# Kernel tuning notes

Measured on AMD Instinct MI355X. Metric: run time of the kernel, lower is better.

The kernel has to match this reference:

```python
import jax, jax.numpy as jnp
import numpy as np

B, T, D = 4, 2048, 1024
H = 16
HD = D // H  # 64


def setup_inputs() -> dict:
    key = jax.random.key(0)
    ks = jax.random.split(key, 6)
    s = 0.02
    x = jax.random.normal(ks[0], (B, T, D), dtype=jnp.float32)
    # per-head projection weights, stored stacked: [H, HD, D] (torch Linear weight layout)
    Wq = jax.random.normal(ks[1], (H, HD, D), dtype=jnp.float32) * s
    Wk = jax.random.normal(ks[2], (H, HD, D), dtype=jnp.float32) * s
    Wv = jax.random.normal(ks[3], (H, HD, D), dtype=jnp.float32) * s
    Wo = jax.random.normal(ks[4], (D, D), dtype=jnp.float32) * s  # proj weight [out, in]
    bo = jax.random.normal(ks[5], (D,), dtype=jnp.float32) * s
    return {"x": x, "Wq": Wq, "Wk": Wk, "Wv": Wv, "Wo": Wo, "bo": bo}


def reference(x, Wq, Wk, Wv, Wo, bo):
    Bx, Tx, _ = x.shape
    # project: [B,T,D] x [H,HD,D] -> [B,H,T,HD]
    q = jnp.einsum('btd,hed->bhte', x, Wq)
    k = jnp.einsum('btd,hed->bhte', x, Wk)
    v = jnp.einsum('btd,hed->bhte', x, Wv)
    scale = 1.0 / jnp.sqrt(jnp.array(q.shape[-1], dtype=x.dtype))
    scores = jnp.einsum('bhte,bhse->bhts', q, k) * scale  # [B,H,T,T]
    causal = jnp.tril(jnp.ones((Tx, Tx), dtype=bool))
    scores = jnp.where(causal, scores, jnp.array(-jnp.inf, dtype=scores.dtype))
    weights = jax.nn.softmax(scores, axis=-1)
    out = jnp.einsum('bhts,bhse->bhte', weights, v)  # [B,H,T,HD]
    # concat heads (head h occupies contiguous slice, matching torch.cat order)
    out = out.transpose(0, 2, 1, 3).reshape(Bx, Tx, -1)  # [B,T,D]
    out = out @ Wo.T + bo
    return out
```

## Files before the change

kernel.cpp:

```cpp
#include <hip/hip_runtime.h>
#include <cstdint>
#include <cstddef>

typedef unsigned short u16;
typedef float  f32x4  __attribute__((ext_vector_type(4)));
typedef __bf16 bf16x8 __attribute__((ext_vector_type(8)));
typedef unsigned short us8 __attribute__((ext_vector_type(8)));
typedef unsigned short us4 __attribute__((ext_vector_type(4)));
typedef float  f32x4v __attribute__((ext_vector_type(4)));

#define AS1 __attribute__((address_space(1)))
#define AS3 __attribute__((address_space(3)))

__device__ __forceinline__ u16 f2b(float f) {
  unsigned u = __float_as_uint(f);
  u += 0x7FFFu + ((u >> 16) & 1u);
  return (u16)(u >> 16);
}

__device__ __forceinline__ bf16x8 ldfrag(const u16* p) {
  us8 v = *(const us8*)p;
  return __builtin_bit_cast(bf16x8, v);
}

__device__ __forceinline__ f32x4 mfma16(bf16x8 a, bf16x8 b, f32x4 c) {
  return __builtin_amdgcn_mfma_f32_16x16x32_bf16(a, b, c, 0, 0, 0);
}

__device__ __forceinline__ void gl_lds16(const u16* g, AS3 u16* l) {
  __builtin_amdgcn_global_load_lds((AS1 void*)g, (AS3 void*)l, 16, 0, 0);
}

__global__ __launch_bounds__(256) void cvt_bf16(const float* __restrict__ s,
                                                u16* __restrict__ d, int n4) {
  int i = blockIdx.x * 256 + threadIdx.x;
  if (i >= n4) return;
  f32x4v f = ((const f32x4v*)s)[i];
  us4 o = { f2b(f[0]), f2b(f[1]), f2b(f[2]), f2b(f[3]) };
  ((us4*)d)[i] = o;
}

__global__ __launch_bounds__(256) void gemm_qkv(
    const u16* __restrict__ A, const u16* __restrict__ W,
    u16* __restrict__ Qb, u16* __restrict__ Kb, u16* __restrict__ Vt) {
  __shared__ u16 lA[128 * 32];
  __shared__ u16 lB[128 * 32];
  const int tid = threadIdx.x;
  const int lane = tid & 63, wave = tid >> 6;
  const int quad = lane >> 4, l16 = lane & 15;
  const int wr = wave >> 1, wc = wave & 1;
  const int m0 = blockIdx.y * 128;
  const int n0 = blockIdx.x * 128;
  const int sec = n0 >> 10;
  AS3 u16* lA3 = (AS3 u16*)lA;
  AS3 u16* lB3 = (AS3 u16*)lB;
  f32x4 acc[4][4] = {};
  const int c0 = tid, c1 = tid + 256;
  const int ar0 = m0 + (c0 >> 2), ac0 = (c0 & 3) * 8;
  const int ar1 = m0 + (c1 >> 2), ac1 = (c1 & 3) * 8;
  const int br0 = n0 + (c0 >> 2);
  const int br1 = n0 + (c1 >> 2);

  for (int k0 = 0; k0 < 1024; k0 += 32) {
    __syncthreads();
    gl_lds16(A + (size_t)ar0 * 1024 + k0 + ac0, lA3 + wave * 512);
    gl_lds16(A + (size_t)ar1 * 1024 + k0 + ac1, lA3 + 2048 + wave * 512);
    gl_lds16(W + (size_t)br0 * 1024 + k0 + ac0, lB3 + wave * 512);
    gl_lds16(W + (size_t)br1 * 1024 + k0 + ac1, lB3 + 2048 + wave * 512);
    __syncthreads();
    bf16x8 aF[4], bF[4];
#pragma unroll
    for (int mt = 0; mt < 4; mt++)
      aF[mt] = ldfrag(&lA[(wr * 64 + mt * 16 + l16) * 32 + quad * 8]);
#pragma unroll
    for (int nt = 0; nt < 4; nt++)
      bF[nt] = ldfrag(&lB[(wc * 64 + nt * 16 + l16) * 32 + quad * 8]);
    if (sec != 2) {
#pragma unroll
      for (int mt = 0; mt < 4; mt++)
#pragma unroll
        for (int nt = 0; nt < 4; nt++)
          acc[mt][nt] = mfma16(aF[mt], bF[nt], acc[mt][nt]);
    } else {
#pragma unroll
      for (int mt = 0; mt < 4; mt++)
#pragma unroll
        for (int nt = 0; nt < 4; nt++)
          acc[mt][nt] = mfma16(bF[nt], aF[mt], acc[mt][nt]);
    }
  }

  if (sec != 2) {
#pragma unroll
    for (int mt = 0; mt < 4; mt++) {
#pragma unroll
      for (int nt = 0; nt < 4; nt++) {
#pragma unroll
        for (int r = 0; r < 4; r++) {
          float v = acc[mt][nt][r];
          int m = m0 + wr * 64 + mt * 16 + quad * 4 + r;
          int n = n0 + wc * 64 + nt * 16 + l16;
          int ns = n & 1023;
          int h = ns >> 6, e = ns & 63;
          int b = m >> 11, t = m & 2047;
          size_t bh = (size_t)b * 16 + h;
          if (sec == 0) Qb[(bh * 2048 + t) * 64 + e] = f2b(v * 0.125f);
          else          Kb[(bh * 2048 + t) * 64 + e] = f2b(v);
        }
      }
    }
  } else {
#pragma unroll
    for (int mt = 0; mt < 4; mt++) {
#pragma unroll
      for (int nt = 0; nt < 4; nt++) {
#pragma unroll
        for (int r = 0; r < 4; r++) {
          float v = acc[mt][nt][r];
          int n = n0 + wc * 64 + nt * 16 + quad * 4 + r;
          int m = m0 + wr * 64 + mt * 16 + l16;
          int ns = n & 1023;
          int h = ns >> 6, e = ns & 63;
          int b = m >> 11, t = m & 2047;
          size_t bh = (size_t)b * 16 + h;
          Vt[(bh * 64 + e) * 2048 + t] = f2b(v);
        }
      }
    }
  }
}

__global__ __launch_bounds__(512, 4) void attn(
    const u16* __restrict__ Q, const u16* __restrict__ K,
    const u16* __restrict__ Vt, u16* __restrict__ O) {
  __shared__ u16 lK[128 * 72];
  __shared__ u16 lV[64 * 136];
  __shared__ u16 lP[8 * 16 * 40];
  const int tid = threadIdx.x;
  const int lane = tid & 63, wave = tid >> 6;
  const int quad = lane >> 4, l16 = lane & 15;
  const int bh = blockIdx.x;
  const int qb = 15 - (int)blockIdx.y;
  const int t0 = qb << 7;
  const size_t base = (size_t)bh * (2048 * 64);
  u16* lPw = lP + wave * 640;

  const int tq = t0 + wave * 16 + l16;
  const bf16x8 qF0 = ldfrag(Q + base + (size_t)tq * 64 + quad * 8);
  const bf16x8 qF1 = ldfrag(Q + base + (size_t)tq * 64 + 32 + quad * 8);

  float m_i = -INFINITY, l_i = 0.f;
  f32x4 o[4] = {};

  for (int j = 0; j <= qb; j++) {
    const int s0 = j << 7;
    __syncthreads();
#pragma unroll
    for (int i = 0; i < 2; i++) {
      int c = tid + i * 512;
      int r = c >> 3, col = (c & 7) * 8;
      *(us8*)&lK[r * 72 + col] = *(const us8*)(K + base + (size_t)(s0 + r) * 64 + col);
    }
#pragma unroll
    for (int i = 0; i < 2; i++) {
      int c = tid + i * 512;
      int e = c >> 4, col = (c & 15) * 8;
      *(us8*)&lV[e * 136 + col] = *(const us8*)(Vt + base + (size_t)e * 2048 + s0 + col);
    }
    __syncthreads();

    f32x4 S[8];
#pragma unroll
    for (int nt = 0; nt < 8; nt++) {
      int sr = nt * 16 + l16;
      f32x4 a = {};
      a = mfma16(ldfrag(&lK[sr * 72 + quad * 8]), qF0, a);
      a = mfma16(ldfrag(&lK[sr * 72 + 32 + quad * 8]), qF1, a);
      S[nt] = a;
    }

    if (j == qb) {
#pragma unroll
      for (int nt = 0; nt < 8; nt++)
#pragma unroll
        for (int r = 0; r < 4; r++) {
          int s = s0 + nt * 16 + quad * 4 + r;
          if (s > tq) S[nt][r] = -INFINITY;
        }
    }

    f32x4 m4 = S[0];
#pragma unroll
    for (int nt = 1; nt < 8; nt++)
#pragma unroll
      for (int r = 0; r < 4; r++) m4[r] = fmaxf(m4[r], S[nt][r]);
    float mx = fmaxf(fmaxf(m4[0], m4[1]), fmaxf(m4[2], m4[3]));
    mx = fmaxf(mx, __shfl_xor(mx, 16));
    mx = fmaxf(mx, __shfl_xor(mx, 32));
    float mn = fmaxf(m_i, mx);
    float alpha = exp2f((m_i - mn) * 1.44269504f);
    float sum = 0.f;
#pragma unroll
    for (int nt = 0; nt < 8; nt++)
#pragma unroll
      for (int r = 0; r < 4; r++) {
        float p = exp2f((S[nt][r] - mn) * 1.44269504f);
        S[nt][r] = p;
        sum += p;
      }
    sum += __shfl_xor(sum, 16);
    sum += __shfl_xor(sum, 32);
    l_i = l_i * alpha + sum;
    m_i = mn;
#pragma unroll
    for (int ot = 0; ot < 4; ot++)
#pragma unroll
      for (int r = 0; r < 4; r++) o[ot][r] *= alpha;

#pragma unroll
    for (int c = 0; c < 4; c++) {
      us4 p0 = { f2b(S[2*c][0]),   f2b(S[2*c][1]),   f2b(S[2*c][2]),   f2b(S[2*c][3]) };
      us4 p1 = { f2b(S[2*c+1][0]), f2b(S[2*c+1][1]), f2b(S[2*c+1][2]), f2b(S[2*c+1][3]) };
      *(us4*)&lPw[l16 * 40 + quad * 4]      = p0;
      *(us4*)&lPw[l16 * 40 + 16 + quad * 4] = p1;
      __asm__ volatile("s_waitcnt lgkmcnt(0)" ::: "memory");
      bf16x8 bP = ldfrag(&lPw[l16 * 40 + quad * 8]);
#pragma unroll
      for (int ot = 0; ot < 4; ot++)
        o[ot] = mfma16(ldfrag(&lV[(ot * 16 + l16) * 136 + c * 32 + quad * 8]), bP, o[ot]);
    }
  }

  const float inv = 1.f / l_i;
  const int b = bh >> 4, h = bh & 15;
#pragma unroll
  for (int ot = 0; ot < 4; ot++) {
    us4 pk = { f2b(o[ot][0] * inv), f2b(o[ot][1] * inv),
               f2b(o[ot][2] * inv), f2b(o[ot][3] * inv) };
    *(us4*)&O[((size_t)b * 2048 + tq) * 1024 + h * 64 + ot * 16 + quad * 4] = pk;
  }
}

__global__ __launch_bounds__(256) void gemm_out(
    const u16* __restrict__ A, const u16* __restrict__ W,
    const float* __restrict__ bias, float* __restrict__ out) {
  __shared__ u16 lA[128 * 32];
  __shared__ u16 lB[128 * 32];
  const int tid = threadIdx.x;
  const int lane = tid & 63, wave = tid >> 6;
  const int quad = lane >> 4, l16 = lane & 15;
  const int wr = wave >> 1, wc = wave & 1;
  const int m0 = blockIdx.y * 128;
  const int n0 = blockIdx.x * 128;
  AS3 u16* lA3 = (AS3 u16*)lA;
  AS3 u16* lB3 = (AS3 u16*)lB;
  f32x4 acc[4][4] = {};
  const int c0 = tid, c1 = tid + 256;
  const int ar0 = m0 + (c0 >> 2), ac0 = (c0 & 3) * 8;
  const int ar1 = m0 + (c1 >> 2), ac1 = (c1 & 3) * 8;
  const int br0 = n0 + (c0 >> 2);
  const int br1 = n0 + (c1 >> 2);

  for (int k0 = 0; k0 < 1024; k0 += 32) {
    __syncthreads();
    gl_lds16(A + (size_t)ar0 * 1024 + k0 + ac0, lA3 + wave * 512);
    gl_lds16(A + (size_t)ar1 * 1024 + k0 + ac1, lA3 + 2048 + wave * 512);
    gl_lds16(W + (size_t)br0 * 1024 + k0 + ac0, lB3 + wave * 512);
    gl_lds16(W + (size_t)br1 * 1024 + k0 + ac1, lB3 + 2048 + wave * 512);
    __syncthreads();
    bf16x8 aF[4], bF[4];
#pragma unroll
    for (int mt = 0; mt < 4; mt++)
      aF[mt] = ldfrag(&lA[(wr * 64 + mt * 16 + l16) * 32 + quad * 8]);
#pragma unroll
    for (int nt = 0; nt < 4; nt++)
      bF[nt] = ldfrag(&lB[(wc * 64 + nt * 16 + l16) * 32 + quad * 8]);
#pragma unroll
    for (int mt = 0; mt < 4; mt++)
#pragma unroll
      for (int nt = 0; nt < 4; nt++)
        acc[mt][nt] = mfma16(aF[mt], bF[nt], acc[mt][nt]);
  }

#pragma unroll
  for (int mt = 0; mt < 4; mt++) {
#pragma unroll
    for (int nt = 0; nt < 4; nt++) {
#pragma unroll
      for (int r = 0; r < 4; r++) {
        int m = m0 + wr * 64 + mt * 16 + quad * 4 + r;
        int n = n0 + wc * 64 + nt * 16 + l16;
        out[(size_t)m * 1024 + n] = acc[mt][nt][r] + bias[n];
      }
    }
  }
}

extern "C" void kernel_launch(void* const* d_in, const int* in_sizes, int n_in,
                              void* d_out, int out_size, void* d_ws, size_t ws_size,
                              hipStream_t stream) {
  const float* x  = (const float*)d_in[0];
  const float* Wq = (const float*)d_in[1];
  const float* Wk = (const float*)d_in[2];
  const float* Wv = (const float*)d_in[3];
  const float* Wo = (const float*)d_in[4];
  const float* bo = (const float*)d_in[5];
  float* out = (float*)d_out;

  u16* ws   = (u16*)d_ws;
  u16* xb   = ws;
  u16* Wqkv = ws + 8388608;
  u16* Wob  = ws + 11534336;
  u16* Qb   = ws + 12582912;
  u16* Ao   = xb;
  u16* Kb   = (u16*)d_out;
  u16* Vt   = Kb + 8388608;

  cvt_bf16<<<8192, 256, 0, stream>>>(x, xb, 2097152);
  cvt_bf16<<<1024, 256, 0, stream>>>(Wq, Wqkv,            262144);
  cvt_bf16<<<1024, 256, 0, stream>>>(Wk, Wqkv + 1048576,  262144);
  cvt_bf16<<<1024, 256, 0, stream>>>(Wv, Wqkv + 2097152,  262144);
  cvt_bf16<<<1024, 256, 0, stream>>>(Wo, Wob,             262144);

  gemm_qkv<<<dim3(24, 64), 256, 0, stream>>>(xb, Wqkv, Qb, Kb, Vt);
  attn<<<dim3(64, 16), 512, 0, stream>>>(Qb, Kb, Vt, Ao);
  gemm_out<<<dim3(8, 64), 256, 0, stream>>>(Ao, Wob, bo, out);
}
```

Measured before the change: 290.7 us.

## Pair causal query blocks per CTA, fold log2e into Q, enlarge QKV GEMM tile

The attention kernel now makes each block process two query tiles, qb and 15-qb, so every block does the same amount of causal work and the grid halves. The log2(e) factor is folded into the Q scale so the softmax calls the raw exp2 builtin directly. The P and O bf16 packing switches to a cheaper perm-based round, which rounds half away from zero instead of to nearest even. The QKV GEMM moves to 512 threads with a 256-row M tile so each block shares its W tile across more rows, at the cost of more LDS and registers per block.

```diff
diff --git a/kernel.cpp b/kernel.cpp
--- a/kernel.cpp
+++ b/kernel.cpp
@@ -8,6 +8,7 @@
 typedef unsigned short us8 __attribute__((ext_vector_type(8)));
 typedef unsigned short us4 __attribute__((ext_vector_type(4)));
 typedef float  f32x4v __attribute__((ext_vector_type(4)));
+typedef unsigned int u32x2 __attribute__((ext_vector_type(2)));
 
 #define AS1 __attribute__((address_space(1)))
 #define AS3 __attribute__((address_space(3)))
@@ -16,6 +17,12 @@
   unsigned u = __float_as_uint(f);
   u += 0x7FFFu + ((u >> 16) & 1u);
   return (u16)(u >> 16);
+}
+
+__device__ __forceinline__ unsigned pkbf(float a, float b) {
+  unsigned ua = __float_as_uint(a) + 0x8000u;
+  unsigned ub = __float_as_uint(b) + 0x8000u;
+  return __builtin_amdgcn_perm(ub, ua, 0x07060302u);
 }
 
 __device__ __forceinline__ bf16x8 ldfrag(const u16* p) {
@@ -40,33 +47,30 @@
   ((us4*)d)[i] = o;
 }
 
-__global__ __launch_bounds__(256) void gemm_qkv(
+__global__ __launch_bounds__(512, 4) void gemm_qkv(
     const u16* __restrict__ A, const u16* __restrict__ W,
     u16* __restrict__ Qb, u16* __restrict__ Kb, u16* __restrict__ Vt) {
-  __shared__ u16 lA[128 * 32];
+  __shared__ u16 lA[256 * 32];
   __shared__ u16 lB[128 * 32];
   const int tid = threadIdx.x;
   const int lane = tid & 63, wave = tid >> 6;
   const int quad = lane >> 4, l16 = lane & 15;
   const int wr = wave >> 1, wc = wave & 1;
-  const int m0 = blockIdx.y * 128;
+  const int m0 = blockIdx.y * 256;
   const int n0 = blockIdx.x * 128;
   const int sec = n0 >> 10;
   AS3 u16* lA3 = (AS3 u16*)lA;
   AS3 u16* lB3 = (AS3 u16*)lB;
   f32x4 acc[4][4] = {};
-  const int c0 = tid, c1 = tid + 256;
-  const int ar0 = m0 + (c0 >> 2), ac0 = (c0 & 3) * 8;
-  const int ar1 = m0 + (c1 >> 2), ac1 = (c1 & 3) * 8;
-  const int br0 = n0 + (c0 >> 2);
-  const int br1 = n0 + (c1 >> 2);
+  const int ar0 = m0 + (tid >> 2), ac = (tid & 3) * 8;
+  const int ar1 = ar0 + 128;
+  const int br0 = n0 + (tid >> 2);
 
   for (int k0 = 0; k0 < 1024; k0 += 32) {
     __syncthreads();
-    gl_lds16(A + (size_t)ar0 * 1024 + k0 + ac0, lA3 + wave * 512);
-    gl_lds16(A + (size_t)ar1 * 1024 + k0 + ac1, lA3 + 2048 + wave * 512);
-    gl_lds16(W + (size_t)br0 * 1024 + k0 + ac0, lB3 + wave * 512);
-    gl_lds16(W + (size_t)br1 * 1024 + k0 + ac1, lB3 + 2048 + wave * 512);
+    gl_lds16(A + (size_t)ar0 * 1024 + k0 + ac, lA3 + wave * 512);
+    gl_lds16(A + (size_t)ar1 * 1024 + k0 + ac, lA3 + 4096 + wave * 512);
+    gl_lds16(W + (size_t)br0 * 1024 + k0 + ac, lB3 + wave * 512);
     __syncthreads();
     bf16x8 aF[4], bF[4];
 #pragma unroll
@@ -91,6 +95,7 @@
   }
 
   if (sec != 2) {
+    const float qs = 0.180336880111120426f;
 #pragma unroll
     for (int mt = 0; mt < 4; mt++) {
 #pragma unroll
@@ -104,7 +109,7 @@
           int h = ns >> 6, e = ns & 63;
           int b = m >> 11, t = m & 2047;
           size_t bh = (size_t)b * 16 + h;
-          if (sec == 0) Qb[(bh * 2048 + t) * 64 + e] = f2b(v * 0.125f);
+          if (sec == 0) Qb[(bh * 2048 + t) * 64 + e] = f2b(v * qs);
           else          Kb[(bh * 2048 + t) * 64 + e] = f2b(v);
         }
       }
@@ -135,109 +140,111 @@
     const u16* __restrict__ Vt, u16* __restrict__ O) {
   __shared__ u16 lK[128 * 72];
   __shared__ u16 lV[64 * 136];
-  __shared__ u16 lP[8 * 16 * 40];
+  __shared__ u16 lP[8 * 16 * 48];
   const int tid = threadIdx.x;
   const int lane = tid & 63, wave = tid >> 6;
   const int quad = lane >> 4, l16 = lane & 15;
   const int bh = blockIdx.x;
-  const int qb = 15 - (int)blockIdx.y;
-  const int t0 = qb << 7;
+  const int pidx = blockIdx.y;
   const size_t base = (size_t)bh * (2048 * 64);
-  u16* lPw = lP + wave * 640;
-
-  const int tq = t0 + wave * 16 + l16;
-  const bf16x8 qF0 = ldfrag(Q + base + (size_t)tq * 64 + quad * 8);
-  const bf16x8 qF1 = ldfrag(Q + base + (size_t)tq * 64 + 32 + quad * 8);
-
-  float m_i = -INFINITY, l_i = 0.f;
-  f32x4 o[4] = {};
-
-  for (int j = 0; j <= qb; j++) {
-    const int s0 = j << 7;
-    __syncthreads();
-#pragma unroll
-    for (int i = 0; i < 2; i++) {
-      int c = tid + i * 512;
-      int r = c >> 3, col = (c & 7) * 8;
-      *(us8*)&lK[r * 72 + col] = *(const us8*)(K + base + (size_t)(s0 + r) * 64 + col);
-    }
-#pragma unroll
-    for (int i = 0; i < 2; i++) {
-      int c = tid + i * 512;
-      int e = c >> 4, col = (c & 15) * 8;
-      *(us8*)&lV[e * 136 + col] = *(const us8*)(Vt + base + (size_t)e * 2048 + s0 + col);
-    }
-    __syncthreads();
-
-    f32x4 S[8];
-#pragma unroll
-    for (int nt = 0; nt < 8; nt++) {
-      int sr = nt * 16 + l16;
-      f32x4 a = {};
-      a = mfma16(ldfrag(&lK[sr * 72 + quad * 8]), qF0, a);
-      a = mfma16(ldfrag(&lK[sr * 72 + 32 + quad * 8]), qF1, a);
-      S[nt] = a;
-    }
-
-    if (j == qb) {
+  u16* lPw = lP + wave * 768;
+  const int b = bh >> 4, h = bh & 15;
+
+  for (int half = 0; half < 2; half++) {
+    const int qb = half ? pidx : (15 - pidx);
+    const int t0 = qb << 7;
+    const int tq = t0 + wave * 16 + l16;
+    const bf16x8 qF0 = ldfrag(Q + base + (size_t)tq * 64 + quad * 8);
+    const bf16x8 qF1 = ldfrag(Q + base + (size_t)tq * 64 + 32 + quad * 8);
+    float m_i = -INFINITY, l_i = 0.f;
+    f32x4 o[4] = {};
+
+    for (int j = 0; j <= qb; j++) {
+      const int s0 = j << 7;
+      __syncthreads();
+#pragma unroll
+      for (int i = 0; i < 2; i++) {
+        int c = tid + i * 512;
+        int r = c >> 3, col = (c & 7) * 8;
+        *(us8*)&lK[r * 72 + col] = *(const us8*)(K + base + (size_t)(s0 + r) * 64 + col);
+      }
+#pragma unroll
+      for (int i = 0; i < 2; i++) {
+        int c = tid + i * 512;
+        int e = c >> 4, col = (c & 15) * 8;
+        *(us8*)&lV[e * 136 + col] = *(const us8*)(Vt + base + (size_t)e * 2048 + s0 + col);
+      }
+      __syncthreads();
+
+      f32x4 S[8];
+#pragma unroll
+      for (int nt = 0; nt < 8; nt++) {
+        int sr = nt * 16 + l16;
+        f32x4 a = {};
+        a = mfma16(ldfrag(&lK[sr * 72 + quad * 8]), qF0, a);
+        a = mfma16(ldfrag(&lK[sr * 72 + 32 + quad * 8]), qF1, a);
+        S[nt] = a;
+      }
+
+      if (j == qb) {
+#pragma unroll
+        for (int nt = 0; nt < 8; nt++)
+#pragma unroll
+          for (int r = 0; r < 4; r++) {
+            int s = s0 + nt * 16 + quad * 4 + r;
+            if (s > tq) S[nt][r] = -INFINITY;
+          }
+      }
+
+      f32x4 m4 = S[0];
+#pragma unroll
+      for (int nt = 1; nt < 8; nt++)
+#pragma unroll
+        for (int r = 0; r < 4; r++) m4[r] = fmaxf(m4[r], S[nt][r]);
+      float mx = fmaxf(fmaxf(m4[0], m4[1]), fmaxf(m4[2], m4[3]));
+      mx = fmaxf(mx, __shfl_xor(mx, 16));
+      mx = fmaxf(mx, __shfl_xor(mx, 32));
+      float mn = fmaxf(m_i, mx);
+      float alpha = __builtin_amdgcn_exp2f(m_i - mn);
+      float sum = 0.f;
 #pragma unroll
       for (int nt = 0; nt < 8; nt++)
 #pragma unroll
         for (int r = 0; r < 4; r++) {
-          int s = s0 + nt * 16 + quad * 4 + r;
-          if (s > tq) S[nt][r] = -INFINITY;
+          float p = __builtin_amdgcn_exp2f(S[nt][r] - mn);
+          S[nt][r] = p;
+          sum += p;
         }
-    }
-
-    f32x4 m4 = S[0];
-#pragma unroll
-    for (int nt = 1; nt < 8; nt++)
-#pragma unroll
-      for (int r = 0; r < 4; r++) m4[r] = fmaxf(m4[r], S[nt][r]);
-    float mx = fmaxf(fmaxf(m4[0], m4[1]), fmaxf(m4[2], m4[3]));
-    mx = fmaxf(mx, __shfl_xor(mx, 16));
-    mx = fmaxf(mx, __shfl_xor(mx, 32));
-    float mn = fmaxf(m_i, mx);
-    float alpha = exp2f((m_i - mn) * 1.44269504f);
-    float sum = 0.f;
-#pragma unroll
-    for (int nt = 0; nt < 8; nt++)
-#pragma unroll
-      for (int r = 0; r < 4; r++) {
-        float p = exp2f((S[nt][r] - mn) * 1.44269504f);
-        S[nt][r] = p;
-        sum += p;
-      }
-    sum += __shfl_xor(sum, 16);
-    sum += __shfl_xor(sum, 32);
-    l_i = l_i * alpha + sum;
-    m_i = mn;
-#pragma unroll
-    for (int ot = 0; ot < 4; ot++)
-#pragma unroll
-      for (int r = 0; r < 4; r++) o[ot][r] *= alpha;
-
-#pragma unroll
-    for (int c = 0; c < 4; c++) {
-      us4 p0 = { f2b(S[2*c][0]),   f2b(S[2*c][1]),   f2b(S[2*c][2]),   f2b(S[2*c][3]) };
-      us4 p1 = { f2b(S[2*c+1][0]), f2b(S[2*c+1][1]), f2b(S[2*c+1][2]), f2b(S[2*c+1][3]) };
-      *(us4*)&lPw[l16 * 40 + quad * 4]      = p0;
-      *(us4*)&lPw[l16 * 40 + 16 + quad * 4] = p1;
-      __asm__ volatile("s_waitcnt lgkmcnt(0)" ::: "memory");
-      bf16x8 bP = ldfrag(&lPw[l16 * 40 + quad * 8]);
+      sum += __shfl_xor(sum, 16);
+      sum += __shfl_xor(sum, 32);
+      l_i = l_i * alpha + sum;
+      m_i = mn;
 #pragma unroll
       for (int ot = 0; ot < 4; ot++)
-        o[ot] = mfma16(ldfrag(&lV[(ot * 16 + l16) * 136 + c * 32 + quad * 8]), bP, o[ot]);
-    }
-  }
-
-  const float inv = 1.f / l_i;
-  const int b = bh >> 4, h = bh & 15;
-#pragma unroll
-  for (int ot = 0; ot < 4; ot++) {
-    us4 pk = { f2b(o[ot][0] * inv), f2b(o[ot][1] * inv),
-               f2b(o[ot][2] * inv), f2b(o[ot][3] * inv) };
-    *(us4*)&O[((size_t)b * 2048 + tq) * 1024 + h * 64 + ot * 16 + quad * 4] = pk;
+#pragma unroll
+        for (int r = 0; r < 4; r++) o[ot][r] *= alpha;
+
+#pragma unroll
+      for (int c = 0; c < 4; c++) {
+        u32x2 d0 = { pkbf(S[2*c][0],   S[2*c][1]),   pkbf(S[2*c][2],   S[2*c][3]) };
+        u32x2 d1 = { pkbf(S[2*c+1][0], S[2*c+1][1]), pkbf(S[2*c+1][2], S[2*c+1][3]) };
+        *(u32x2*)&lPw[l16 * 48 + quad * 4]      = d0;
+        *(u32x2*)&lPw[l16 * 48 + 16 + quad * 4] = d1;
+        __asm__ volatile("s_waitcnt lgkmcnt(0)" ::: "memory");
+        bf16x8 bP = ldfrag(&lPw[l16 * 48 + quad * 8]);
+#pragma unroll
+        for (int ot = 0; ot < 4; ot++)
+          o[ot] = mfma16(ldfrag(&lV[(ot * 16 + l16) * 136 + c * 32 + quad * 8]), bP, o[ot]);
+      }
+    }
+
+    const float inv = 1.f / l_i;
+#pragma unroll
+    for (int ot = 0; ot < 4; ot++) {
+      u32x2 pk = { pkbf(o[ot][0] * inv, o[ot][1] * inv),
+                   pkbf(o[ot][2] * inv, o[ot][3] * inv) };
+      *(u32x2*)&O[((size_t)b * 2048 + tq) * 1024 + h * 64 + ot * 16 + quad * 4] = pk;
+    }
   }
 }
 
@@ -322,7 +329,7 @@
   cvt_bf16<<<1024, 256, 0, stream>>>(Wv, Wqkv + 2097152,  262144);
   cvt_bf16<<<1024, 256, 0, stream>>>(Wo, Wob,             262144);
 
-  gemm_qkv<<<dim3(24, 64), 256, 0, stream>>>(xb, Wqkv, Qb, Kb, Vt);
-  attn<<<dim3(64, 16), 512, 0, stream>>>(Qb, Kb, Vt, Ao);
+  gemm_qkv<<<dim3(24, 32), 512, 0, stream>>>(xb, Wqkv, Qb, Kb, Vt);
+  attn<<<dim3(64, 8), 512, 0, stream>>>(Qb, Kb, Vt, Ao);
   gemm_out<<<dim3(8, 64), 256, 0, stream>>>(Ao, Wob, bo, out);
 }
```

Result: slower. 761.4 us (+161.9%).
